# Optimization experiments

Hardware: AMD Instinct MI355X
Metric: run time of the kernel (lower is better)

Reference implementation:

```python
import jax, jax.numpy as jnp
import numpy as np
from jax import lax

EPS = 1e-5

def _conv_bn(x, w, b, g, be, stride, pad, alpha=0.1):
    # x: [N, Cin, L]; w: [Cout, Cin, K]
    y = lax.conv_general_dilated(x, w, (stride,), [(pad, pad)],
                                 dimension_numbers=('NCH', 'OIH', 'NCH'))
    y = y + b[None, :, None]
    y = jnp.where(y > 0, y, alpha * y)  # LeakyReLU(0.1)
    # BatchNorm1d, training-mode batch stats over (N, L)
    mu = jnp.mean(y, axis=(0, 2), keepdims=True)
    var = jnp.var(y, axis=(0, 2), keepdims=True)
    y = (y - mu) * lax.rsqrt(var + EPS)
    return y * g[None, :, None] + be[None, :, None]

def _forward(x, c, emb, w1, b1, g1, be1, w2, b2, g2, be2, w3, b3, g3, be3,
             w4, b4, g4, be4, w5, b5, g5, be5, fcW, fcb, memK, memV):
    B, S = x.shape
    D = 512  # lstm_size * 32
    e = emb[x]                       # [B, S, 256]
    cf = c.reshape(B * S, c.shape[2])
    ce = emb[cf]                     # [B*S, ctx_len, 256]
    h = _conv_bn(ce, w1, b1, g1, be1, 2, 2)
    h = _conv_bn(h, w2, b2, g2, be2, 2, 2)
    h = _conv_bn(h, w3, b3, g3, be3, 2, 2)
    h = _conv_bn(h, w4, b4, g4, be4, 2, 2)
    h = _conv_bn(h, w5, b5, g5, be5, 1, 0)   # [B*S, 512, 1]
    cfeat = h.reshape(B, S, D)
    # DatabaseMemory: content attention over external DB (vectorized over all
    # 32 per-step slices at once; the original Python loop is stateless per-slice)
    scores = jnp.einsum('bsd,md->bsm', cfeat, memK) / jnp.sqrt(jnp.asarray(D, cfeat.dtype))
    attn = jax.nn.softmax(scores, axis=-1)
    m_out = jnp.einsum('bsm,md->bsd', attn, memV)  # [B, S, 512]
    s = jnp.concatenate([e, cfeat, m_out], axis=2)  # [B, S, 1280]
    logits = jax.nn.softmax(s @ fcW + fcb, axis=2)  # [B, S, vocab]
    return logits

def setup_inputs() -> dict:
    key = jax.random.key(0)
    ks = jax.random.split(key, 12)
    B, S, CTX, V, E = 32, 32, 64, 32000, 256
    d = {}
    d['x'] = jax.random.randint(ks[0], (B, S), 0, V)
    d['c'] = jax.random.randint(ks[1], (B, S, CTX), 0, V)
    d['emb'] = jax.random.normal(ks[2], (V, E), jnp.float32) * 0.02
    convs = [(32, CTX, 8), (64, 32, 8), (128, 64, 8), (256, 128, 8), (512, 256, 14)]
    for i, (co, ci, k) in enumerate(convs, 1):
        kk = jax.random.fold_in(ks[3], i)
        scale = (2.0 / (ci * k)) ** 0.5
        d[f'w{i}'] = jax.random.normal(kk, (co, ci, k), jnp.float32) * scale
        d[f'b{i}'] = jnp.zeros((co,), jnp.float32)
        d[f'g{i}'] = jnp.ones((co,), jnp.float32)
        d[f'be{i}'] = jnp.zeros((co,), jnp.float32)
    d['fcW'] = jax.random.normal(ks[4], (1280, V), jnp.float32) * (1.0 / 1280 ** 0.5)
    d['fcb'] = jnp.zeros((V,), jnp.float32)
    d['memK'] = jax.random.normal(ks[5], (4096, 512), jnp.float32) * 0.05
    d['memV'] = jax.random.normal(ks[6], (4096, 512), jnp.float32) * 0.05
    return d

def reference(x, c, emb, w1, b1, g1, be1, w2, b2, g2, be2, w3, b3, g3, be3,
              w4, b4, g4, be4, w5, b5, g5, be5, fcW, fcb, memK, memV):
    return _forward(x, c, emb, w1, b1, g1, be1, w2, b2, g2, be2, w3, b3, g3,
                    be3, w4, b4, g4, be4, w5, b5, g5, be5, fcW, fcb, memK, memV)
```

## Files before the change

kernel.cpp:

```cpp
#include <hip/hip_runtime.h>
#include <hip/hip_bf16.h>
#include <math.h>


#define N_SAMP 1024

typedef __bf16 bf16x8 __attribute__((ext_vector_type(8)));
typedef __bf16 bf16x4 __attribute__((ext_vector_type(4)));
typedef float  f32x4  __attribute__((ext_vector_type(4)));

__device__ __forceinline__ float blockReduceMax256(float v) {
    __shared__ float sm[4];
    #pragma unroll
    for (int off = 32; off > 0; off >>= 1) v = fmaxf(v, __shfl_down(v, off, 64));
    if ((threadIdx.x & 63) == 0) sm[threadIdx.x >> 6] = v;
    __syncthreads();
    v = fmaxf(fmaxf(sm[0], sm[1]), fmaxf(sm[2], sm[3]));
    __syncthreads();
    return v;
}

__device__ __forceinline__ float blockReduceSum256(float v) {
    __shared__ float sm[4];
    #pragma unroll
    for (int off = 32; off > 0; off >>= 1) v += __shfl_down(v, off, 64);
    if ((threadIdx.x & 63) == 0) sm[threadIdx.x >> 6] = v;
    __syncthreads();
    v = sm[0] + sm[1] + sm[2] + sm[3];
    __syncthreads();
    return v;
}

__global__ __launch_bounds__(256)
void gather_tr_kernel(const int* __restrict__ Cidx, const float* __restrict__ Emb,
                      __bf16* __restrict__ Gt) {
    const int n = blockIdx.x;
    __shared__ int idx[64];
    __shared__ float t[64][65];
    if (threadIdx.x < 64) idx[threadIdx.x] = Cidx[n * 64 + threadIdx.x];
    __bf16* g = Gt + (size_t)n * (262 * 64);
    for (int i = threadIdx.x; i < 6 * 64; i += 256) {
        int r = i >> 6;
        int phys = (r < 2) ? r : r + 256;
        g[(size_t)phys * 64 + (i & 63)] = (__bf16)0.f;
    }
    for (int c0 = 0; c0 < 256; c0 += 64) {
        __syncthreads();
        for (int i = threadIdx.x; i < 4096; i += 256) {
            int ci = i >> 6, li = i & 63;
            t[ci][li] = Emb[(size_t)idx[ci] * 256 + c0 + li];
        }
        __syncthreads();
        for (int i = threadIdx.x; i < 4096; i += 256) {
            int li = i >> 6, ci = i & 63;
            g[(size_t)(2 + c0 + li) * 64 + ci] = (__bf16)t[ci][li];
        }
    }
}

__global__ __launch_bounds__(256)
void wt_fold_kernel(const float* __restrict__ W, const float* __restrict__ B,
                    const float* __restrict__ SS, __bf16* __restrict__ Wt,
                    float* __restrict__ bias, int CO, int CI, int KW) {
    const int co = blockIdx.x;
    const int K = CI * KW;
    float local = 0.f;
    if (co < CO) {
        for (int i = threadIdx.x; i < K; i += 256) {
            int k = i / CI, ci = i - k * CI;
            float w = W[((size_t)co * CI + ci) * KW + k];
            float sc = SS ? SS[ci] : 1.f;
            Wt[(size_t)co * K + i] = (__bf16)(w * sc);
            if (SS) local = fmaf(SS[CI + ci], w, local);
        }
    } else {
        for (int i = threadIdx.x; i < K; i += 256)
            Wt[(size_t)co * K + i] = (__bf16)0.f;
    }
    __shared__ float sm[4];
    #pragma unroll
    for (int off = 32; off > 0; off >>= 1) local += __shfl_down(local, off, 64);
    if ((threadIdx.x & 63) == 0) sm[threadIdx.x >> 6] = local;
    __syncthreads();
    if (threadIdx.x == 0 && co < CO)
        bias[co] = B[co] + sm[0] + sm[1] + sm[2] + sm[3];
}

__global__ __launch_bounds__(256)
void padfill_kernel(__bf16* __restrict__ Y, const float* __restrict__ SS,
                    int C, int LSTR, int4 rows, int nrows) {
    const int n = blockIdx.x;
    const int rr[4] = {rows.x, rows.y, rows.z, rows.w};
    for (int i = threadIdx.x; i < nrows * C; i += 256) {
        int j = i / C, c = i - j * C;
        float p = -SS[C + c] / SS[c];
        Y[((size_t)n * LSTR + rr[j]) * C + c] = (__bf16)p;
    }
}

template<int C, int LOUT, int LSTR, int NB>
__global__ __launch_bounds__(256)
void bn_stats_bf_kernel(const __bf16* __restrict__ Y, float2* __restrict__ partial) {
    constexpr int RPT = 256 / C;
    constexpr int M = N_SAMP * LOUT;
    const int col = threadIdx.x & (C - 1);
    const int rofs = threadIdx.x / C;
    float s = 0.f, s2 = 0.f;
    for (int m = blockIdx.x * RPT + rofs; m < M; m += NB * RPT) {
        int n = m / LOUT, l = m - n * LOUT;
        float v = (float)Y[((size_t)n * LSTR + 2 + l) * C + col];
        s += v; s2 = fmaf(v, v, s2);
    }
    __shared__ float sm[256], sm2[256];
    sm[threadIdx.x] = s; sm2[threadIdx.x] = s2;
    __syncthreads();
    #pragma unroll
    for (int off = 128; off >= C; off >>= 1) {
        if (threadIdx.x < off) {
            sm[threadIdx.x] += sm[threadIdx.x + off];
            sm2[threadIdx.x] += sm2[threadIdx.x + off];
        }
        __syncthreads();
    }
    if (threadIdx.x < C)
        partial[(size_t)blockIdx.x * C + threadIdx.x] =
            make_float2(sm[threadIdx.x], sm2[threadIdx.x]);
}

__global__ __launch_bounds__(256)
void bn_stats_cf_kernel(const float* __restrict__ Y, float2* __restrict__ partial) {
    const int n0 = blockIdx.x * 4;
    for (int c = threadIdx.x; c < 512; c += 256) {
        float s = 0.f, s2 = 0.f;
        #pragma unroll
        for (int r = 0; r < 4; r++) {
            float v = Y[(size_t)(n0 + r) * 512 + c];
            s += v; s2 = fmaf(v, v, s2);
        }
        partial[(size_t)blockIdx.x * 512 + c] = make_float2(s, s2);
    }
}

__global__ __launch_bounds__(64)
void bn_finalize_kernel(const float2* __restrict__ partial,
                        const float* __restrict__ G, const float* __restrict__ Be,
                        float* __restrict__ SS, int C, int NB, float invCnt) {
    const int c = blockIdx.x;
    float s = 0.f, s2 = 0.f;
    for (int i = threadIdx.x; i < NB; i += 64) {
        float2 p = partial[(size_t)i * C + c];
        s += p.x; s2 += p.y;
    }
    #pragma unroll
    for (int off = 32; off > 0; off >>= 1) {
        s  += __shfl_down(s,  off, 64);
        s2 += __shfl_down(s2, off, 64);
    }
    if (threadIdx.x == 0) {
        double mu  = (double)s * invCnt;
        double var = (double)s2 * invCnt - mu * mu;
        float sc = (float)((double)G[c] / sqrt(var + 1e-5));
        SS[c] = sc;
        SS[C + c] = (float)((double)Be[c] - mu * sc);
    }
}

__device__ __forceinline__ void gld16(const __bf16* g, __bf16* l) {
    __builtin_amdgcn_global_load_lds(
        (const __attribute__((address_space(1))) unsigned int*)g,
        (__attribute__((address_space(3))) unsigned int*)l, 16, 0, 0);
}

__global__ __launch_bounds__(256)
void mfma_gemm_bt(const __bf16* __restrict__ A, const __bf16* __restrict__ B,
                  const float* __restrict__ bias, void* __restrict__ Cv,
                  int N, int K, int ksplit,
                  int lda, int lda2, int rpbl, long long ablk,
                  int ldc2, long long csplit,
                  float scale, int leaky, int swz, int cdt) {
    __shared__ __bf16 As[128 * 32];
    __shared__ __bf16 Bs[128 * 32];
    const int tid = threadIdx.x;
    int bx = blockIdx.x, by = blockIdx.y;
    if (swz) {
        const int gx = gridDim.x;
        const int G = gx * gridDim.y;
        const int bid = by * gx + bx;
        const int fid = (bid & 7) * (G >> 3) + (bid >> 3);
        bx = fid % gx; by = fid / gx;
    }
    const int col0 = by * 128;
    const int rpbm = (1 << rpbl) - 1;

    const int r  = tid >> 2;
    const int kb = (((tid & 3) ^ ((tid >> 3) & 3))) * 8;
    const int r1 = r + 64;
    const __bf16* Ab = A + (size_t)bx * ablk;
    const __bf16* Ag0 = Ab + (size_t)(r  >> rpbl) * lda2 + (size_t)(r  & rpbm) * lda + kb;
    const __bf16* Ag1 = Ab + (size_t)(r1 >> rpbl) * lda2 + (size_t)(r1 & rpbm) * lda + kb;
    const __bf16* Bg0 = B + (size_t)(col0 + r ) * K + kb;
    const __bf16* Bg1 = B + (size_t)(col0 + r1) * K + kb;
    __bf16* Al0 = As + tid * 8;
    __bf16* Al1 = As + 2048 + tid * 8;
    __bf16* Bl0 = Bs + tid * 8;
    __bf16* Bl1 = Bs + 2048 + tid * 8;

    const int lane = tid & 63;
    const int wave = tid >> 6;
    const int wy = wave >> 1, wx = wave & 1;
    const int l15 = lane & 15, quad = lane >> 4;
    const int xq = (quad ^ ((l15 >> 1) & 3)) * 8;

    f32x4 acc[4][4] = {};

    const int k0s = blockIdx.z * ksplit;
    const int k0e = k0s + ksplit;
    for (int k0 = k0s; k0 < k0e; k0 += 32) {
        __syncthreads();
        gld16(Ag0 + k0, Al0);
        gld16(Ag1 + k0, Al1);
        gld16(Bg0 + k0, Bl0);
        gld16(Bg1 + k0, Bl1);
        __syncthreads();

        bf16x8 af[4], bfr[4];
        #pragma unroll
        for (int mi = 0; mi < 4; mi++)
            af[mi] = *(const bf16x8*)&As[(wy * 64 + mi * 16 + l15) * 32 + xq];
        #pragma unroll
        for (int ni = 0; ni < 4; ni++)
            bfr[ni] = *(const bf16x8*)&Bs[(wx * 64 + ni * 16 + l15) * 32 + xq];
        #pragma unroll
        for (int mi = 0; mi < 4; mi++)
            #pragma unroll
            for (int ni = 0; ni < 4; ni++)
                acc[mi][ni] = __builtin_amdgcn_mfma_f32_16x16x32_bf16(
                    af[mi], bfr[ni], acc[mi][ni], 0, 0, 0);
    }

    const long long cb = (long long)blockIdx.z * csplit
                       + (long long)bx * (long long)((128 >> rpbl) * ldc2);
    #pragma unroll
    for (int mi = 0; mi < 4; mi++) {
        #pragma unroll
        for (int ni = 0; ni < 4; ni++) {
            const int col = col0 + wx * 64 + ni * 16 + l15;
            if (col < N) {
                const float bv = bias ? bias[col] : 0.f;
                #pragma unroll
                for (int rg = 0; rg < 4; rg++) {
                    const int row = wy * 64 + mi * 16 + quad * 4 + rg;
                    const long long a = cb + (long long)(row >> rpbl) * ldc2
                                      + (long long)(row & rpbm) * N + col;
                    float t = acc[mi][ni][rg] * scale + bv;
                    if (leaky) t = t > 0.f ? t : 0.1f * t;
                    if (cdt) ((__bf16*)Cv)[a] = (__bf16)t;
                    else     ((float*)Cv)[a] = t;
                }
            }
        }
    }
}

__global__ __launch_bounds__(256)
void splitk_reduce_kernel(const float* __restrict__ P, float* __restrict__ out,
                          const float* __restrict__ bias, int S, int MN, int N,
                          int leaky) {
    int i = blockIdx.x * 256 + threadIdx.x;
    const int tot = MN >> 2;
    if (i >= tot) return;
    float ax = 0.f, ay = 0.f, az = 0.f, aw = 0.f;
    for (int s = 0; s < S; s++) {
        float4 p = ((const float4*)(P + (size_t)s * MN))[i];
        ax += p.x; ay += p.y; az += p.z; aw += p.w;
    }
    const int c0 = (i * 4) & (N - 1);
    float4 o;
    o.x = ax + (bias ? bias[c0 + 0] : 0.f);
    o.y = ay + (bias ? bias[c0 + 1] : 0.f);
    o.z = az + (bias ? bias[c0 + 2] : 0.f);
    o.w = aw + (bias ? bias[c0 + 3] : 0.f);
    if (leaky) {
        o.x = o.x > 0.f ? o.x : 0.1f * o.x;
        o.y = o.y > 0.f ? o.y : 0.1f * o.y;
        o.z = o.z > 0.f ? o.z : 0.1f * o.z;
        o.w = o.w > 0.f ? o.w : 0.1f * o.w;
    }
    ((float4*)out)[i] = o;
}

__global__ __launch_bounds__(256)
void cast_bf16_kernel(const float* __restrict__ in, __bf16* __restrict__ out, int n8) {
    int i = blockIdx.x * 256 + threadIdx.x;
    if (i >= n8) return;
    float4 a = ((const float4*)in)[2 * i];
    float4 b = ((const float4*)in)[2 * i + 1];
    bf16x8 v;
    v[0] = (__bf16)a.x; v[1] = (__bf16)a.y; v[2] = (__bf16)a.z; v[3] = (__bf16)a.w;
    v[4] = (__bf16)b.x; v[5] = (__bf16)b.y; v[6] = (__bf16)b.z; v[7] = (__bf16)b.w;
    ((bf16x8*)out)[i] = v;
}

__global__ __launch_bounds__(256)
void bn_apply_both_kernel(float* __restrict__ Y, __bf16* __restrict__ Yb,
                          const float* __restrict__ SS, int n4) {
    int i = blockIdx.x * 256 + threadIdx.x;
    if (i >= n4) return;
    float4 v = ((float4*)Y)[i];
    const int c = (i * 4) & 511;
    v.x = fmaf(v.x, SS[c + 0], SS[512 + c + 0]);
    v.y = fmaf(v.y, SS[c + 1], SS[512 + c + 1]);
    v.z = fmaf(v.z, SS[c + 2], SS[512 + c + 2]);
    v.w = fmaf(v.w, SS[c + 3], SS[512 + c + 3]);
    ((float4*)Y)[i] = v;
    bf16x4 o;
    o[0] = (__bf16)v.x; o[1] = (__bf16)v.y; o[2] = (__bf16)v.z; o[3] = (__bf16)v.w;
    ((bf16x4*)Yb)[i] = o;
}

__global__ __launch_bounds__(256)
void transpose_cast_kernel(const float* __restrict__ in, __bf16* __restrict__ out,
                           int R, int C) {
    __shared__ float t[32][33];
    const int c0 = blockIdx.x * 32, r0 = blockIdx.y * 32;
    const int cc = threadIdx.x & 31, rr = threadIdx.x >> 5;
    #pragma unroll
    for (int i = 0; i < 32; i += 8)
        t[rr + i][cc] = in[(size_t)(r0 + rr + i) * C + c0 + cc];
    __syncthreads();
    #pragma unroll
    for (int i = 0; i < 32; i += 8)
        out[(size_t)(c0 + rr + i) * R + r0 + cc] = (__bf16)t[cc][rr + i];
}

__global__ __launch_bounds__(256)
void softmax4k_kernel(float* __restrict__ P) {
    float* p = P + (size_t)blockIdx.x * 4096;
    float v[16];
    float mx = -INFINITY;
    #pragma unroll
    for (int i = 0; i < 16; i++) {
        v[i] = p[threadIdx.x + i * 256];
        mx = fmaxf(mx, v[i]);
    }
    mx = blockReduceMax256(mx);
    float s = 0.f;
    #pragma unroll
    for (int i = 0; i < 16; i++) { v[i] = __expf(v[i] - mx); s += v[i]; }
    s = blockReduceSum256(s);
    const float inv = 1.f / s;
    #pragma unroll
    for (int i = 0; i < 16; i++) p[threadIdx.x + i * 256] = v[i] * inv;
}

__global__ __launch_bounds__(256)
void softmax_fc_kernel(float* __restrict__ P) {
    float* p = P + (size_t)blockIdx.x * 32000;
    float m = -INFINITY, s = 0.f;
    for (int i = threadIdx.x; i < 32000; i += 256) {
        float v = p[i];
        if (v > m) { s = s * __expf(m - v) + 1.f; m = v; }
        else       { s += __expf(v - m); }
    }
    const float M = blockReduceMax256(m);
    s *= __expf(m - M);
    const float S = blockReduceSum256(s);
    const float inv = 1.f / S;
    for (int i = threadIdx.x; i < 32000; i += 256)
        p[i] = __expf(p[i] - M) * inv;
}

__global__ __launch_bounds__(320)
void assemble_s_kernel(const int* __restrict__ X, const float* __restrict__ Emb,
                       const float* __restrict__ Cf, const float* __restrict__ Mo,
                       __bf16* __restrict__ S) {
    const int m = blockIdx.x;
    const int col = threadIdx.x * 4;
    float4 v;
    if (col < 256)      v = *(const float4*)(Emb + (size_t)X[m] * 256 + col);
    else if (col < 768) v = *(const float4*)(Cf + (size_t)m * 512 + (col - 256));
    else                v = *(const float4*)(Mo + (size_t)m * 512 + (col - 768));
    bf16x4 o;
    o[0] = (__bf16)v.x; o[1] = (__bf16)v.y; o[2] = (__bf16)v.z; o[3] = (__bf16)v.w;
    *(bf16x4*)(S + (size_t)m * 1280 + col) = o;
}

extern "C" void kernel_launch(void* const* d_in, const int* in_sizes, int n_in,
                              void* d_out, int out_size, void* d_ws, size_t ws_size,
                              hipStream_t stream) {
    const int*   x    = (const int*)d_in[0];
    const int*   c    = (const int*)d_in[1];
    const float* emb  = (const float*)d_in[2];
    const float* w1 = (const float*)d_in[3],  *b1 = (const float*)d_in[4];
    const float* g1 = (const float*)d_in[5],  *be1 = (const float*)d_in[6];
    const float* w2 = (const float*)d_in[7],  *b2 = (const float*)d_in[8];
    const float* g2 = (const float*)d_in[9],  *be2 = (const float*)d_in[10];
    const float* w3 = (const float*)d_in[11], *b3 = (const float*)d_in[12];
    const float* g3 = (const float*)d_in[13], *be3 = (const float*)d_in[14];
    const float* w4 = (const float*)d_in[15], *b4 = (const float*)d_in[16];
    const float* g4 = (const float*)d_in[17], *be4 = (const float*)d_in[18];
    const float* w5 = (const float*)d_in[19], *b5 = (const float*)d_in[20];
    const float* g5 = (const float*)d_in[21], *be5 = (const float*)d_in[22];
    const float* fcW = (const float*)d_in[23], *fcb = (const float*)d_in[24];
    const float* memK = (const float*)d_in[25], *memV = (const float*)d_in[26];
    float* out = (float*)d_out;

    char* W = (char*)d_ws;
    __bf16* fcWT_bf  = (__bf16*)(W + 0);
    __bf16* memK_bf  = (__bf16*)(W + 81920000);
    __bf16* memVT_bf = (__bf16*)(W + 86114304);
    __bf16* w5t      = (__bf16*)(W + 90308608);
    __bf16* w4t      = (__bf16*)(W + 93978624);
    __bf16* w3t      = (__bf16*)(W + 94502912);
    __bf16* w2t      = (__bf16*)(W + 94633984);
    __bf16* w1t      = (__bf16*)(W + 94699520);
    float*  SS       = (float*)(W + 94830592);
    float*  BB       = (float*)(W + 94834688);
    float2* part     = (float2*)(W + 94836736);
    __bf16* YA = (__bf16*)(W + 95885312);
    __bf16* YB = (__bf16*)(W + 104814592);
    char* P = W + 114268160;
    __bf16* Gt      = (__bf16*)P;
    float*  Pc5     = (float*)P;
    float*  scores  = (float*)P;
    __bf16* attn_bf = (__bf16*)(P + 16777216);
    float*  Pmo     = (float*)(P + 25165824);
    float*  cfeat    = (float*)(W + 148609024);
    __bf16* cfeat_bf = (__bf16*)(W + 150706176);
    float*  m_out    = (float*)(W + 151754752);
    __bf16* s_bf     = (__bf16*)(W + 153851904);

    __bf16* Y1 = YA; __bf16* Y3 = YA;
    __bf16* Y2 = YB; __bf16* Y4 = YB;

    transpose_cast_kernel<<<dim3(1000, 40), 256, 0, stream>>>(fcW, fcWT_bf, 1280, 32000);
    transpose_cast_kernel<<<dim3(16, 128), 256, 0, stream>>>(memV, memVT_bf, 4096, 512);
    cast_bf16_kernel<<<1024, 256, 0, stream>>>(memK, memK_bf, 262144);
    wt_fold_kernel<<<128, 256, 0, stream>>>(w1, b1, nullptr, w1t, BB, 32, 64, 8);
    gather_tr_kernel<<<1024, 256, 0, stream>>>(c, emb, Gt);

    mfma_gemm_bt<<<dim3(1024, 1), 256, 0, stream>>>(Gt, w1t, BB, Y1 + 64,
        32, 512, 512, 128, 0, 7, 16768LL, 4160, 0LL, 1.0f, 1, 0, 1);
    bn_stats_bf_kernel<32, 127, 130, 512><<<512, 256, 0, stream>>>(Y1, part);
    bn_finalize_kernel<<<32, 64, 0, stream>>>(part, g1, be1, SS, 32, 512,
                                              1.0f / (1024.f * 127.f));
    padfill_kernel<<<1024, 256, 0, stream>>>(Y1, SS, 32, 130,
                                             make_int4(0, 1, 129, 0), 3);
    wt_fold_kernel<<<128, 256, 0, stream>>>(w2, b2, SS, w2t, BB, 64, 32, 8);

    mfma_gemm_bt<<<dim3(512, 1), 256, 0, stream>>>(Y1, w2t, BB, Y2 + 128,
        64, 256, 256, 64, 4160, 6, 8320LL, 4224, 0LL, 1.0f, 1, 0, 1);
    bn_stats_bf_kernel<64, 62, 66, 256><<<256, 256, 0, stream>>>(Y2, part);
    bn_finalize_kernel<<<64, 64, 0, stream>>>(part, g2, be2, SS, 64, 256,
                                              1.0f / (1024.f * 62.f));
    padfill_kernel<<<1024, 256, 0, stream>>>(Y2, SS, 64, 66,
                                             make_int4(0, 1, 64, 65), 4);
    wt_fold_kernel<<<128, 256, 0, stream>>>(w3, b3, SS, w3t, BB, 128, 64, 8);

    mfma_gemm_bt<<<dim3(256, 1), 256, 0, stream>>>(Y2, w3t, BB, Y3 + 256,
        128, 512, 512, 128, 4224, 5, 16896LL, 4352, 0LL, 1.0f, 1, 0, 1);
    bn_stats_bf_kernel<128, 30, 34, 256><<<256, 256, 0, stream>>>(Y3, part);
    bn_finalize_kernel<<<128, 64, 0, stream>>>(part, g3, be3, SS, 128, 256,
                                               1.0f / (1024.f * 30.f));
    padfill_kernel<<<1024, 256, 0, stream>>>(Y3, SS, 128, 34,
                                             make_int4(0, 1, 32, 33), 4);
    wt_fold_kernel<<<256, 256, 0, stream>>>(w4, b4, SS, w4t, BB, 256, 128, 8);

    mfma_gemm_bt<<<dim3(128, 2), 256, 0, stream>>>(Y3, w4t, BB, Y4 + 512,
        256, 1024, 1024, 256, 4352, 4, 34816LL, 4608, 0LL, 1.0f, 1, 0, 1);
    bn_stats_bf_kernel<256, 14, 18, 256><<<256, 256, 0, stream>>>(Y4, part);
    bn_finalize_kernel<<<256, 64, 0, stream>>>(part, g4, be4, SS, 256, 256,
                                               1.0f / (1024.f * 14.f));
    wt_fold_kernel<<<512, 256, 0, stream>>>(w5, b5, SS, w5t, BB, 512, 256, 14);

    mfma_gemm_bt<<<dim3(8, 4, 8), 256, 0, stream>>>(Y4 + 512, w5t, nullptr, Pc5,
        512, 3584, 448, 4608, 0, 7, 589824LL, 65536, 524288LL, 1.0f, 0, 0, 0);
    splitk_reduce_kernel<<<512, 256, 0, stream>>>(Pc5, cfeat, BB, 8, 524288, 512, 1);
    bn_stats_cf_kernel<<<256, 256, 0, stream>>>(cfeat, part);
    bn_finalize_kernel<<<512, 64, 0, stream>>>(part, g5, be5, SS, 512, 256,
                                               1.0f / 1024.f);
    bn_apply_both_kernel<<<512, 256, 0, stream>>>(cfeat, cfeat_bf, SS, 131072);

    mfma_gemm_bt<<<dim3(8, 32), 256, 0, stream>>>(cfeat_bf, memK_bf, nullptr, scores,
        4096, 512, 512, 512, 0, 7, 65536LL, 524288, 0LL,
        0.04419417382415922f, 0, 1, 0);
    softmax4k_kernel<<<1024, 256, 0, stream>>>(scores);
    cast_bf16_kernel<<<2048, 256, 0, stream>>>(scores, attn_bf, 524288);
    mfma_gemm_bt<<<dim3(8, 4, 4), 256, 0, stream>>>(attn_bf, memVT_bf, nullptr, Pmo,
        512, 4096, 1024, 4096, 0, 7, 524288LL, 65536, 524288LL, 1.0f, 0, 0, 0);
    splitk_reduce_kernel<<<512, 256, 0, stream>>>(Pmo, m_out, nullptr, 4, 524288, 512, 0);

    assemble_s_kernel<<<1024, 320, 0, stream>>>(x, emb, cfeat, m_out, s_bf);
    mfma_gemm_bt<<<dim3(8, 250), 256, 0, stream>>>(s_bf, fcWT_bf, fcb, out,
        32000, 1280, 1280, 1280, 0, 7, 163840LL, 4096000, 0LL, 1.0f, 0, 1, 0);
    softmax_fc_kernel<<<1024, 256, 0, stream>>>(out);
}
```

Before: 950.3 us.

## Add 256x256-tile double-buffered MFMA GEMM for final vocab projection

Introduces a new 512-thread GEMM kernel with 256x256 output tiles, double-buffered LDS staging via direct global-to-LDS loads, XOR-swizzled LDS layout, interleaved fragment loads and MFMA with priority hints, and XCD-aware block remapping. It replaces the previous 128-tile GEMM for the 1024x32000x1280 logits projection, aiming to raise data reuse and MFMA utilisation. Larger tiles mean fewer blocks (500) and higher register/LDS pressure, and the kernel assumes M, N divisible by 256 and K by 64.

Result: no change. 933.2 us (-1.8%).

```diff
diff --git a/kernel.cpp b/kernel.cpp
--- a/kernel.cpp
+++ b/kernel.cpp
@@ -257,6 +257,145 @@
                     if (cdt) ((__bf16*)Cv)[a] = (__bf16)t;
                     else     ((float*)Cv)[a] = t;
                 }
+            }
+        }
+    }
+}
+
+#define SBAR() do { __builtin_amdgcn_sched_barrier(0); \
+                    __builtin_amdgcn_s_barrier(); \
+                    __builtin_amdgcn_sched_barrier(0); } while (0)
+
+#define LDA256(mb) do { \
+    _Pragma("unroll") \
+    for (int m_ = 0; m_ < 4; m_++) \
+        _Pragma("unroll") \
+        for (int k_ = 0; k_ < 2; k_++) \
+            afr[mb][m_][k_] = *(const bf16x8*)&Asl[((mb) * 64 + m_ * 16) * 64 + \
+                ((((k_) << 2) + quad) ^ rotA) * 8]; \
+} while (0)
+
+#define LDB256(nb) do { \
+    _Pragma("unroll") \
+    for (int n_ = 0; n_ < 2; n_++) \
+        _Pragma("unroll") \
+        for (int k_ = 0; k_ < 2; k_++) \
+            bfr[nb][n_][k_] = *(const bf16x8*)&Bsl[((nb) * 32 + n_ * 16) * 64 + \
+                ((((k_) << 2) + quad) ^ rotB) * 8]; \
+} while (0)
+
+#define MM256(mb, nb) do { \
+    _Pragma("unroll") \
+    for (int m_ = 0; m_ < 4; m_++) \
+        _Pragma("unroll") \
+        for (int n_ = 0; n_ < 2; n_++) \
+            _Pragma("unroll") \
+            for (int k_ = 0; k_ < 2; k_++) \
+                acc[(mb) * 4 + m_][(nb) * 2 + n_] = \
+                    __builtin_amdgcn_mfma_f32_16x16x32_bf16( \
+                        afr[mb][m_][k_], bfr[nb][n_][k_], \
+                        acc[(mb) * 4 + m_][(nb) * 2 + n_], 0, 0, 0); \
+} while (0)
+
+#define STG256(ko, bb) do { \
+    const size_t ko_ = (size_t)(ko); \
+    gld16(Ab + ko_,            AldsB + (bb) * 16384); \
+    gld16(Ab + ko_ +     giK,  AldsB + (bb) * 16384 + 4096); \
+    gld16(Ab + ko_ + 2 * giK,  AldsB + (bb) * 16384 + 8192); \
+    gld16(Ab + ko_ + 3 * giK,  AldsB + (bb) * 16384 + 12288); \
+    gld16(Bb + ko_,            BldsB + (bb) * 16384); \
+    gld16(Bb + ko_ +     giK,  BldsB + (bb) * 16384 + 4096); \
+    gld16(Bb + ko_ + 2 * giK,  BldsB + (bb) * 16384 + 8192); \
+    gld16(Bb + ko_ + 3 * giK,  BldsB + (bb) * 16384 + 12288); \
+} while (0)
+
+__global__ __launch_bounds__(512, 2)
+void mfma_gemm256_bt(const __bf16* __restrict__ A, const __bf16* __restrict__ B,
+                     const float* __restrict__ bias, float* __restrict__ C,
+                     int M, int N, int K, int nwg) {
+    __shared__ __bf16 As2[2 * 16384];
+    __shared__ __bf16 Bs2[2 * 16384];
+    const int tid = threadIdx.x;
+
+    const int bid = blockIdx.x;
+    const int q8 = nwg >> 3, r8 = nwg & 7;
+    const int xcd = bid & 7, o8 = bid >> 3;
+    const int fid = (xcd < r8 ? xcd * (q8 + 1) : r8 * (q8 + 1) + (xcd - r8) * q8) + o8;
+    const int gx = M >> 8;
+    const int bx = fid % gx, by = fid / gx;
+    const int row0 = bx << 8, col0 = by << 8;
+
+    const int lane = tid & 63;
+    const int wave = tid >> 6;
+    const int wr = wave >> 2, wc = wave & 3;
+    const int l15 = lane & 15, quad = lane >> 4;
+
+    const int rloc = tid >> 3;
+    const int sq   = tid & 7;
+    const int ksel = (sq ^ (rloc & 7)) << 3;
+    const __bf16* Ab = A + (size_t)(row0 + rloc) * K + ksel;
+    const __bf16* Bb = B + (size_t)(col0 + rloc) * K + ksel;
+    __bf16* AldsB = As2 + tid * 8;
+    __bf16* BldsB = Bs2 + tid * 8;
+    const size_t giK = (size_t)64 * K;
+
+    const int arow = wr * 128 + l15;
+    const int brow = wc * 64 + l15;
+    const int rotA = arow & 7, rotB = brow & 7;
+
+    f32x4 acc[8][4] = {};
+    bf16x8 afr[2][4][2];
+    bf16x8 bfr[2][2][2];
+
+    const int NT = K >> 6;
+    STG256(0, 0);
+
+    for (int t = 0; t < NT; ++t) {
+        const int cb = t & 1;
+        if (t + 1 < NT) {
+            STG256((size_t)(t + 1) * 64, cb ^ 1);
+            asm volatile("s_waitcnt vmcnt(8)" ::: "memory");
+        } else {
+            asm volatile("s_waitcnt vmcnt(0)" ::: "memory");
+        }
+        SBAR();
+
+        const __bf16* Asl = As2 + cb * 16384 + arow * 64;
+        const __bf16* Bsl = Bs2 + cb * 16384 + brow * 64;
+
+        LDA256(0);
+        LDB256(0);
+        SBAR();
+        LDB256(1);
+        __builtin_amdgcn_s_setprio(1);
+        MM256(0, 0);
+        __builtin_amdgcn_s_setprio(0);
+        SBAR();
+        LDA256(1);
+        __builtin_amdgcn_s_setprio(1);
+        MM256(0, 1);
+        __builtin_amdgcn_s_setprio(0);
+        SBAR();
+        __builtin_amdgcn_s_setprio(1);
+        MM256(1, 0);
+        __builtin_amdgcn_s_setprio(0);
+        SBAR();
+        __builtin_amdgcn_s_setprio(1);
+        MM256(1, 1);
+        __builtin_amdgcn_s_setprio(0);
+        SBAR();
+    }
+
+    #pragma unroll
+    for (int mi = 0; mi < 8; mi++) {
+        #pragma unroll
+        for (int ni = 0; ni < 4; ni++) {
+            const int colv = col0 + wc * 64 + ni * 16 + l15;
+            const float bv = bias ? bias[colv] : 0.f;
+            #pragma unroll
+            for (int rg = 0; rg < 4; rg++) {
+                const int row = row0 + wr * 128 + mi * 16 + quad * 4 + rg;
+                C[(size_t)row * N + colv] = acc[mi][ni][rg] + bv;
             }
         }
     }
@@ -491,7 +630,7 @@
     splitk_reduce_kernel<<<512, 256, 0, stream>>>(Pmo, m_out, nullptr, 4, 524288, 512, 0);
 
     assemble_s_kernel<<<1024, 320, 0, stream>>>(x, emb, cfeat, m_out, s_bf);
-    mfma_gemm_bt<<<dim3(8, 250), 256, 0, stream>>>(s_bf, fcWT_bf, fcb, out,
-        32000, 1280, 1280, 1280, 0, 7, 163840LL, 4096000, 0LL, 1.0f, 0, 1, 0);
+    mfma_gemm256_bt<<<dim3(500), 512, 0, stream>>>(s_bf, fcWT_bf, fcb, out,
+                                                   1024, 32000, 1280, 500);
     softmax_fc_kernel<<<1024, 256, 0, stream>>>(out);
 }
```
